# Optimization experiments

Measured on AMD Instinct MI355X. Metric: run time of the kernel, lower is better.

Reference implementation:

```python
import jax, jax.numpy as jnp
import numpy as np

N_NODES = 100000
N_EDGES = 1600000
NEG_SLOPE = 0.2
EPS = 1e-6


def setup_inputs() -> dict:
    key = jax.random.key(0)
    ks = jax.random.split(key, 14)
    s = 0.1  # weight init scale
    return {
        "x": jax.random.normal(ks[0], (N_NODES, 64), jnp.float32),
        "src": jax.random.randint(ks[1], (N_EDGES,), 0, N_NODES, jnp.int32),
        "dst": jax.random.randint(ks[2], (N_EDGES,), 0, N_NODES, jnp.int32),
        "W0": s * jax.random.normal(ks[3], (64, 128), jnp.float32),
        "al0": s * jax.random.normal(ks[4], (4, 32), jnp.float32),
        "ar0": s * jax.random.normal(ks[5], (4, 32), jnp.float32),
        "W1": s * jax.random.normal(ks[6], (128, 128), jnp.float32),
        "al1": s * jax.random.normal(ks[7], (4, 32), jnp.float32),
        "ar1": s * jax.random.normal(ks[8], (4, 32), jnp.float32),
        "resW1": s * jax.random.normal(ks[9], (128, 128), jnp.float32),
        "W2": s * jax.random.normal(ks[10], (128, 32), jnp.float32),
        "al2": s * jax.random.normal(ks[11], (1, 32), jnp.float32),
        "ar2": s * jax.random.normal(ks[12], (1, 32), jnp.float32),
        "resW2": s * jax.random.normal(ks[13], (128, 32), jnp.float32),
    }


def gat_conv(h, src, dst, W, al, ar, resW):
    """DGL-style GATConv. h: [N, Fin]; returns [N, H, D]."""
    H, D = al.shape
    feat = (h @ W).reshape(-1, H, D)                       # [N,H,D]
    el = jnp.sum(feat * al, axis=-1)                       # [N,H]
    er = jnp.sum(feat * ar, axis=-1)                       # [N,H]
    e = jax.nn.leaky_relu(el[src] + er[dst], NEG_SLOPE)    # [E,H]
    # segment softmax over destination nodes
    m = jax.ops.segment_max(e, dst, num_segments=N_NODES)  # [N,H]
    ex = jnp.exp(e - m[dst])                               # [E,H]
    denom = jax.ops.segment_sum(ex, dst, num_segments=N_NODES)
    alpha = ex / denom[dst]                                # [E,H]
    msg = alpha[:, :, None] * feat[src]                    # [E,H,D]
    rst = jax.ops.segment_sum(msg, dst, num_segments=N_NODES)  # [N,H,D]
    if resW is not None:
        rst = rst + (h @ resW).reshape(-1, H, D)
    return rst


def pairnorm_scs(x, scale=1.0):
    # 'PN-SCS' mode: scale-individually then center by original column mean
    col_mean = jnp.mean(x, axis=0)
    rownorm = jnp.sqrt(EPS + jnp.sum(x * x, axis=1, keepdims=True))
    return scale * x / rownorm - col_mean


def reference(x, src, dst, W0, al0, ar0, W1, al1, ar1, resW1, W2, al2, ar2, resW2):
    # layer 0: no residual, activation applied outside
    h = gat_conv(x, src, dst, W0, al0, ar0, None)          # [N,4,32]
    h = jax.nn.elu(h.reshape(h.shape[0], -1))              # [N,128]
    h = pairnorm_scs(h)
    # middle layer: residual + internal ELU (DGL applies activation inside),
    # then the outer loop flattens and applies ELU again
    h = jax.nn.elu(gat_conv(h, src, dst, W1, al1, ar1, resW1))  # [N,4,32]
    h = jax.nn.elu(h.reshape(h.shape[0], -1))              # [N,128]
    h = pairnorm_scs(h)
    # final layer: residual, mean over heads
    h = gat_conv(h, src, dst, W2, al2, ar2, resW2)         # [N,1,32]
    h = jnp.mean(h, axis=1)                                # [N,32]
    # dgl.mean_nodes readout on a single graph -> mean over nodes
    return jnp.mean(h, axis=0)                             # [32]
```

## Files before the change

kernel.cpp:

```cpp
#include <hip/hip_runtime.h>


typedef __attribute__((ext_vector_type(8))) short s8v;
typedef __attribute__((ext_vector_type(4))) float f4v;
typedef __attribute__((ext_vector_type(2))) float f2v;
typedef __attribute__((ext_vector_type(2))) _Float16 h2;
typedef __attribute__((ext_vector_type(4))) _Float16 h4;

__device__ __forceinline__ unsigned short f2bf(float f) {
  unsigned int x = __float_as_uint(f);
  x += 0x7fffu + ((x >> 16) & 1u);
  return (unsigned short)(x >> 16);
}
__device__ __forceinline__ float bf2f(unsigned short u) {
  return __uint_as_float(((unsigned int)u) << 16);
}
__device__ __forceinline__ unsigned short f2h(float f) {
  _Float16 h = (_Float16)f;
  return __builtin_bit_cast(unsigned short, h);
}
__device__ __forceinline__ unsigned char f2fp8(float v) {
  return (unsigned char)(__builtin_amdgcn_cvt_pk_fp8_f32(v, v, 0, false) & 0xff);
}
__device__ __forceinline__ float lrelu(float x) { return fmaxf(x, 0.2f * x); }
__device__ __forceinline__ float elu1(float x) { return x > 0.f ? x : __expf(x) - 1.f; }

__device__ __forceinline__ void pack_one(const float* W, const float* al, const float* ar,
                                         const float* resW, unsigned short* out,
                                         int K, int M, int BF, int H, int RES0, int t) {
  int c = t / K, k = t - c * K;
  float v = 0.f;
  if (c < BF) {
    v = W[k * BF + c];
  } else if (c < BF + H) {
    int h = c - BF;
    float s = 0.f;
    for (int d = 0; d < 32; d++) s += W[k * BF + h * 32 + d] * al[h * 32 + d];
    v = s;
  } else if (c < BF + 2 * H) {
    int h = c - BF - H;
    float s = 0.f;
    for (int d = 0; d < 32; d++) s += W[k * BF + h * 32 + d] * ar[h * 32 + d];
    v = s;
  } else if (c >= RES0) {
    v = resW[k * (M - RES0) + (c - RES0)];
  }
  unsigned short hi = f2bf(v);
  out[c * K + k] = hi;
  out[M * K + c * K + k] = f2bf(v - bf2f(hi));
}

__global__ __launch_bounds__(256) void hist_pack_k(const int* __restrict__ dst, int* __restrict__ counts,
                                                   int* __restrict__ bhist, int E, int NB, int chunk, int P2B,
                                                   const float* __restrict__ W0, const float* __restrict__ al0,
                                                   const float* __restrict__ ar0,
                                                   const float* __restrict__ W1, const float* __restrict__ al1,
                                                   const float* __restrict__ ar1, const float* __restrict__ resW1,
                                                   const float* __restrict__ W2, const float* __restrict__ al2,
                                                   const float* __restrict__ ar2, const float* __restrict__ resW2,
                                                   unsigned short* __restrict__ w0t, unsigned short* __restrict__ w1t,
                                                   unsigned short* __restrict__ w2t) {
  if ((int)blockIdx.x < P2B) {
    __shared__ int h[512];
    for (int b = threadIdx.x; b < NB; b += 256) h[b] = 0;
    __syncthreads();
    int e0 = blockIdx.x * chunk;
    int e1 = min(E, e0 + chunk);
    for (int e = e0 + threadIdx.x; e < e1; e += 256) {
      int d = dst[e];
      atomicAdd(&counts[d], 1);
      atomicAdd(&h[d >> 8], 1);
    }
    __syncthreads();
    for (int b = threadIdx.x; b < NB; b += 256)
      bhist[(size_t)b * P2B + blockIdx.x] = h[b];
  } else {
    const int n0 = 144 * 64, n1 = 272 * 128, n2 = 80 * 128;
    int t = ((int)blockIdx.x - P2B) * 256 + threadIdx.x;
    if (t < n0) {
      pack_one(W0, al0, ar0, nullptr, w0t, 64, 144, 128, 4, 144, t);
    } else if (t < n0 + n1) {
      pack_one(W1, al1, ar1, resW1, w1t, 128, 272, 128, 4, 144, t - n0);
    } else if (t < n0 + n1 + n2) {
      pack_one(W2, al2, ar2, resW2, w2t, 128, 80, 32, 1, 48, t - n0 - n1);
    }
  }
}

__global__ __launch_bounds__(256) void scanA(const int* __restrict__ counts, int* __restrict__ rsp,
                                             int* __restrict__ bsumA, int* __restrict__ bhist,
                                             int* __restrict__ bsumB, int NA, int NSEG, int nbA) {
  __shared__ int s[256];
  int t = threadIdx.x;
  bool isA = (int)blockIdx.x < nbA;
  int bb = isA ? (int)blockIdx.x : (int)blockIdx.x - nbA;
  const int* in = isA ? counts : bhist;
  int* out = isA ? rsp : bhist;
  int* bs = isA ? bsumA : bsumB;
  int Nn = isA ? NA : NSEG;
  int base = bb * 1024 + t * 4;
  int v0 = (base + 0 < Nn) ? in[base + 0] : 0;
  int v1 = (base + 1 < Nn) ? in[base + 1] : 0;
  int v2 = (base + 2 < Nn) ? in[base + 2] : 0;
  int v3 = (base + 3 < Nn) ? in[base + 3] : 0;
  if (isA) {
    v0 = (v0 + 15) & ~15;
    v1 = (v1 + 15) & ~15;
    v2 = (v2 + 15) & ~15;
    v3 = (v3 + 15) & ~15;
  }
  s[t] = v0 + v1 + v2 + v3;
  __syncthreads();
  for (int off = 1; off < 256; off <<= 1) {
    int xv = (t >= off) ? s[t - off] : 0;
    __syncthreads();
    s[t] += xv;
    __syncthreads();
  }
  int excl = t ? s[t - 1] : 0;
  if (t == 255) bs[bb] = s[255];
  if (base + 0 < Nn) { out[base + 0] = excl; excl += v0; }
  if (base + 1 < Nn) { out[base + 1] = excl; excl += v1; }
  if (base + 2 < Nn) { out[base + 2] = excl; excl += v2; }
  if (base + 3 < Nn) { out[base + 3] = excl; }
}

__global__ __launch_bounds__(256) void scanB(int* __restrict__ rsp, const int* __restrict__ bsumA,
                                             int* __restrict__ bhist, const int* __restrict__ bsumB,
                                             int NA, int NSEG, int nbA, int nbB) {
  __shared__ int s[256];
  int t = threadIdx.x;
  bool isA = (int)blockIdx.x < nbA;
  int bb = isA ? (int)blockIdx.x : (int)blockIdx.x - nbA;
  int* arr = isA ? rsp : bhist;
  const int* bs = isA ? bsumA : bsumB;
  int nb = isA ? nbA : nbB;
  int Nn = isA ? NA : NSEG;
  s[t] = (t < nb) ? bs[t] : 0;
  __syncthreads();
  for (int off = 1; off < 256; off <<= 1) {
    int xv = (t >= off) ? s[t - off] : 0;
    __syncthreads();
    s[t] += xv;
    __syncthreads();
  }
  int pref = bb ? s[bb - 1] : 0;
  if (pref != 0) {
    int base = bb * 1024 + t * 4;
    if (base + 0 < Nn) arr[base + 0] += pref;
    if (base + 1 < Nn) arr[base + 1] += pref;
    if (base + 2 < Nn) arr[base + 2] += pref;
    if (base + 3 < Nn) arr[base + 3] += pref;
  }
}

__global__ __launch_bounds__(256) void bscatter_k(const int* __restrict__ src, const int* __restrict__ dst,
                                                  const int* __restrict__ seg, unsigned int* __restrict__ ebuf,
                                                  int E, int NB, int chunk) {
  __shared__ int cur[512];
  for (int b = threadIdx.x; b < NB; b += 256)
    cur[b] = seg[(size_t)b * gridDim.x + blockIdx.x];
  __syncthreads();
  int e0 = blockIdx.x * chunk;
  int e1 = min(E, e0 + chunk);
  for (int e = e0 + threadIdx.x; e < e1; e += 256) {
    int d = dst[e];
    int pos = atomicAdd(&cur[d >> 8], 1);
    ebuf[pos] = ((unsigned int)src[e] << 8) | (unsigned int)(d & 255);
  }
}

__global__ __launch_bounds__(256) void fscatter_k(const unsigned int* __restrict__ ebuf,
                                                  const int* __restrict__ seg,
                                                  const int* __restrict__ rsp, int* __restrict__ csr_src,
                                                  int E, int NB, int P2B, int Nn) {
  __shared__ int cur[256];
  int b = blockIdx.x;
  int node0 = b << 8;
  int node = node0 + threadIdx.x;
  if (node < Nn) cur[threadIdx.x] = rsp[node];
  __syncthreads();
  int bstart = seg[(size_t)b * P2B];
  int bend = (b + 1 < NB) ? seg[(size_t)(b + 1) * P2B] : E;
  for (int e = bstart + threadIdx.x; e < bend; e += 256) {
    unsigned int sd = ebuf[e];
    int pos = atomicAdd(&cur[sd & 255u], 1);
    csr_src[pos] = (int)(sd >> 8);
  }
}

template <int K, int M, int R, int BF, int H, int RES0, bool AF32, bool CMW>
__global__ __launch_bounds__(256) void gemm_bf16(const void* __restrict__ Av,
                                                 const unsigned short* __restrict__ Bt,
                                                 const float* __restrict__ colsum, float invN,
                                                 unsigned char* __restrict__ feat8,
                                                 float* __restrict__ el, float* __restrict__ er,
                                                 unsigned short* __restrict__ resh, int nRowTiles) {
  __shared__ float cmw_s[M];
  if constexpr (CMW) {
    for (int cc = threadIdx.x; cc < M; cc += 256) {
      float s = 0.f;
      for (int k = 0; k < K; k++)
        s += colsum[k] * (bf2f(Bt[cc * K + k]) + bf2f(Bt[(size_t)M * K + cc * K + k]));
      cmw_s[cc] = s * invN;
    }
    __syncthreads();
  }
  int wv = (int)((blockIdx.x * blockDim.x + threadIdx.x) >> 6);
  int tile0 = wv * R;
  if (tile0 >= nRowTiles) return;
  int lane = threadIdx.x & 63;
  int r = lane & 15, q = lane >> 4;
  s8v afrag[R][K / 32];
#pragma unroll
  for (int rr = 0; rr < R; rr++) {
    if constexpr (AF32) {
      const float* arow = (const float*)Av + (size_t)((tile0 + rr) * 16 + r) * K + q * 8;
#pragma unroll
      for (int kk = 0; kk < K / 32; kk++) {
        s8v v;
#pragma unroll
        for (int j = 0; j < 8; j++) v[j] = (short)f2bf(arow[kk * 32 + j]);
        afrag[rr][kk] = v;
      }
    } else {
      const unsigned short* arow = (const unsigned short*)Av + (size_t)((tile0 + rr) * 16 + r) * K + q * 8;
#pragma unroll
      for (int kk = 0; kk < K / 32; kk++) afrag[rr][kk] = *(const s8v*)(arow + kk * 32);
    }
  }
#pragma unroll
  for (int ct = 0; ct < M / 16; ct++) {
    const unsigned short* brow = Bt + (size_t)(ct * 16 + r) * K + q * 8;
    s8v bhi[K / 32], blo[K / 32];
#pragma unroll
    for (int kk = 0; kk < K / 32; kk++) {
      bhi[kk] = *(const s8v*)(brow + kk * 32);
      blo[kk] = *(const s8v*)(brow + (size_t)M * K + kk * 32);
    }
    int col = ct * 16 + r;
    float cmwv = 0.f;
    if constexpr (CMW) cmwv = cmw_s[col];
#pragma unroll
    for (int rr = 0; rr < R; rr++) {
      f4v acc = {0.f, 0.f, 0.f, 0.f};
#pragma unroll
      for (int kk = 0; kk < K / 32; kk++) {
        acc = __builtin_amdgcn_mfma_f32_16x16x32_bf16(afrag[rr][kk], bhi[kk], acc, 0, 0, 0);
        acc = __builtin_amdgcn_mfma_f32_16x16x32_bf16(afrag[rr][kk], blo[kk], acc, 0, 0, 0);
      }
      int row0 = (tile0 + rr) * 16 + q * 4;
#pragma unroll
      for (int i = 0; i < 4; i++) {
        float v = acc[i] - cmwv;
        size_t row = (size_t)(row0 + i);
        if (col < BF) {
          feat8[row * BF + col] = f2fp8(v);
        } else if (col < BF + H) {
          el[row * H + (col - BF)] = v;
        } else if (col < BF + 2 * H) {
          er[row * H + (col - BF - H)] = v;
        } else if (RES0 < M && col >= RES0) {
          resh[row * (M - RES0) + (col - RES0)] = f2h(v);
        }
      }
    }
  }
}

template <int MODE>
__global__ __launch_bounds__(256) void aggregate4(const unsigned char* __restrict__ feat8,
                                                  const float* __restrict__ el4,
                                                  const float* __restrict__ er4,
                                                  const int* __restrict__ csr_src,
                                                  const int* __restrict__ rsp,
                                                  const int* __restrict__ counts,
                                                  const unsigned short* __restrict__ resh,
                                                  unsigned short* __restrict__ vbf,
                                                  float* __restrict__ rnrm, int Nn) {
  int n = (int)((blockIdx.x * blockDim.x + threadIdx.x) >> 6);
  if (n >= Nn) return;
  int lane = threadIdx.x & 63;
  int start = __builtin_amdgcn_readfirstlane(rsp[n]);
  int deg = __builtin_amdgcn_readfirstlane(counts[n]);
  int chunks = (deg + 15) >> 4;
  int slot = lane >> 2, h = lane & 3;
  float ern = er4[(size_t)n * 4 + h];
  int hl = lane >> 4;
  unsigned dby = (unsigned)lane << 1;
  f2v a01 = {0.f, 0.f};
  float dsum = 0.f;
  float elv = el4[(size_t)csr_src[start + slot] * 4 + h];
  for (int c = 0; c < chunks; c++) {
    const int* csp = csr_src + start + (c << 4);
    int sj[16];
#pragma unroll
    for (int j = 0; j < 16; j++) sj[j] = csp[j];
    float e = elv + ern;
    float exv = (((c << 4) + slot) < deg) ? __expf(fmaxf(e, 0.2f * e)) : 0.f;
    dsum += exv;
    if (c + 1 < chunks) elv = el4[(size_t)csp[16 + slot] * 4 + h];
#pragma unroll
    for (int j = 0; j < 16; j++) {
      float aw = __shfl(exv, (j << 2) | hl);
      unsigned short u = *(const unsigned short*)(feat8 + (((unsigned)sj[j] << 7) + dby));
      f2v fv = __builtin_amdgcn_cvt_pk_f32_fp8((int)u, false);
      f2v aw2 = {aw, aw};
      a01 = __builtin_elementwise_fma(fv, aw2, a01);
    }
  }
#pragma unroll
  for (int off = 4; off < 64; off <<= 1) dsum += __shfl_xor(dsum, off);
  float inv = dsum > 0.f ? 1.f / dsum : 0.f;
  float invh = __shfl(inv, hl);
  float v0, v1;
  if (MODE == 1) {
    h2 rr = *(const h2*)(resh + (size_t)n * 128 + lane * 2);
    v0 = elu1(elu1(a01[0] * invh + (float)rr[0]));
    v1 = elu1(elu1(a01[1] * invh + (float)rr[1]));
  } else {
    v0 = elu1(a01[0] * invh);
    v1 = elu1(a01[1] * invh);
  }
  float ss = v0 * v0 + v1 * v1;
#pragma unroll
  for (int off = 1; off < 64; off <<= 1) ss += __shfl_xor(ss, off);
  float rn = sqrtf(1e-6f + ss);
  float ri = 1.f / rn;
  unsigned int pk = (unsigned int)f2bf(v0 * ri) | ((unsigned int)f2bf(v1 * ri) << 16);
  *(unsigned int*)((char*)vbf + ((size_t)n << 8) + (lane << 2)) = pk;
  if (lane == 0) rnrm[n] = rn;
}

__global__ __launch_bounds__(256) void aggregate1(const unsigned char* __restrict__ feat8,
                                                  const float* __restrict__ el1,
                                                  const float* __restrict__ er1,
                                                  const int* __restrict__ csr_src,
                                                  const int* __restrict__ rsp,
                                                  const int* __restrict__ counts,
                                                  const unsigned short* __restrict__ res2h,
                                                  float* __restrict__ out2, int Nn) {
  int n = (int)((blockIdx.x * blockDim.x + threadIdx.x) >> 6);
  if (n >= Nn) return;
  int lane = threadIdx.x & 63;
  int start = __builtin_amdgcn_readfirstlane(rsp[n]);
  int deg = __builtin_amdgcn_readfirstlane(counts[n]);
  int chunks = (deg + 15) >> 4;
  int l16 = lane & 15;
  float ern = er1[n];
  int g = lane >> 3;
  unsigned dofs4 = (unsigned)(lane & 7) << 2;
  f2v acc01 = {0.f, 0.f}, acc23 = {0.f, 0.f};
  float dsum = 0.f;
  int sA = csr_src[start + l16];
  float elv = el1[sA];
  for (int c = 0; c < chunks; c++) {
    const int* csp = csr_src + start + (c << 4);
    float exv = (((c << 4) + l16) < deg) ? __expf(lrelu(elv + ern)) : 0.f;
    dsum += exv;
    int sAc = sA;
    if (c + 1 < chunks) {
      sA = csp[16 + l16];
      elv = el1[sA];
    }
#pragma unroll
    for (int t = 0; t < 2; t++) {
      int j = (t << 3) + g;
      int sj = __shfl(sAc, j);
      float aw = __shfl(exv, j);
      f2v aw2 = {aw, aw};
      unsigned int u = *(const unsigned int*)(feat8 + (((unsigned)sj << 5) + dofs4));
      f2v fa = __builtin_amdgcn_cvt_pk_f32_fp8((int)u, false);
      f2v fb = __builtin_amdgcn_cvt_pk_f32_fp8((int)u, true);
      acc01 = __builtin_elementwise_fma(fa, aw2, acc01);
      acc23 = __builtin_elementwise_fma(fb, aw2, acc23);
    }
  }
#pragma unroll
  for (int off = 1; off < 16; off <<= 1) dsum += __shfl_xor(dsum, off);
  float inv = dsum > 0.f ? 1.f / dsum : 0.f;
#pragma unroll
  for (int off = 8; off < 64; off <<= 1) {
    acc01[0] += __shfl_xor(acc01[0], off);
    acc01[1] += __shfl_xor(acc01[1], off);
    acc23[0] += __shfl_xor(acc23[0], off);
    acc23[1] += __shfl_xor(acc23[1], off);
  }
  if (lane < 8) {
    h4 rr = *(const h4*)(res2h + (size_t)n * 32 + (lane << 2));
    float4 o;
    o.x = acc01[0] * inv + (float)rr[0];
    o.y = acc01[1] * inv + (float)rr[1];
    o.z = acc23[0] * inv + (float)rr[2];
    o.w = acc23[1] * inv + (float)rr[3];
    *(float4*)(out2 + (size_t)n * 32 + (lane << 2)) = o;
  }
}

__global__ __launch_bounds__(256) void colsum_k(const unsigned short* __restrict__ vbf,
                                                const float* __restrict__ rnrm,
                                                float* __restrict__ colsum, int Nn) {
  __shared__ float ls[256];
  int tid = threadIdx.x;
  int c = tid & 127, rsub = tid >> 7;
  float cs = 0.f;
  for (int r = blockIdx.x * 2 + rsub; r < Nn; r += gridDim.x * 2)
    cs += bf2f(vbf[(size_t)r * 128 + c]) * rnrm[r];
  ls[tid] = cs;
  __syncthreads();
  if (tid < 128) atomicAdd(&colsum[tid], ls[tid] + ls[tid + 128]);
}

__global__ __launch_bounds__(256) void final_reduce(const float* __restrict__ out2,
                                                    float* __restrict__ outsum, int Nn) {
  __shared__ float ls[32];
  if (threadIdx.x < 32) ls[threadIdx.x] = 0.f;
  __syncthreads();
  int d = threadIdx.x & 31, rl = threadIdx.x >> 5;
  float acc = 0.f;
  for (int n = blockIdx.x * 8 + rl; n < Nn; n += gridDim.x * 8)
    acc += out2[(size_t)n * 32 + d];
  atomicAdd(&ls[d], acc);
  __syncthreads();
  if (threadIdx.x < 32) atomicAdd(&outsum[threadIdx.x], ls[threadIdx.x]);
}

__global__ void finalize_k(const float* __restrict__ outsum, float* __restrict__ out, float invN) {
  int t = threadIdx.x;
  if (t < 32) out[t] = outsum[t] * invN;
}

extern "C" void kernel_launch(void* const* d_in, const int* in_sizes, int n_in,
                              void* d_out, int out_size, void* d_ws, size_t ws_size,
                              hipStream_t stream) {
  const float* x     = (const float*)d_in[0];
  const int*   src   = (const int*)d_in[1];
  const int*   dst   = (const int*)d_in[2];
  const float* W0    = (const float*)d_in[3];
  const float* al0   = (const float*)d_in[4];
  const float* ar0   = (const float*)d_in[5];
  const float* W1    = (const float*)d_in[6];
  const float* al1   = (const float*)d_in[7];
  const float* ar1   = (const float*)d_in[8];
  const float* resW1 = (const float*)d_in[9];
  const float* W2    = (const float*)d_in[10];
  const float* al2   = (const float*)d_in[11];
  const float* ar2   = (const float*)d_in[12];
  const float* resW2 = (const float*)d_in[13];
  const int N = in_sizes[0] / 64;
  const int E = in_sizes[1];
  const float invN = 1.f / (float)N;
  const int Emax = E + 15 * N + 1024;
  const int NB = (N + 255) >> 8;
  const int P2B = 512;
  const int chunk = (E + P2B - 1) / P2B;
  const int segN = NB * P2B;
  const int nbA = (N + 1023) / 1024;
  const int nbB = (segN + 1023) / 1024;

  char* p = (char*)d_ws;
  auto alloc = [&](size_t bytes) { char* r = p; p += (bytes + 255) & ~(size_t)255; return r; };

  char* zbase = p;
  int*   counts  = (int*)alloc((size_t)4 * N);
  float* colsumA = (float*)alloc(512);
  float* colsumB = (float*)alloc(512);
  float* outsum  = (float*)alloc(128);
  size_t zbytes = (size_t)(p - zbase);

  int* rsp   = (int*)alloc((size_t)4 * N);
  int* bsumA = (int*)alloc(1024);
  int* bhist = (int*)alloc((size_t)4 * segN);
  int* bsumB = (int*)alloc(1024);
  unsigned int* ebuf = (unsigned int*)alloc((size_t)4 * E);
  int* csr_src = (int*)alloc((size_t)4 * Emax);
  unsigned char*  feat8 = (unsigned char*)alloc((size_t)N * 128);
  unsigned short* vbf   = (unsigned short*)alloc((size_t)2 * N * 128);
  unsigned short* resh  = (unsigned short*)alloc((size_t)2 * N * 128);
  unsigned short* w0t = (unsigned short*)alloc((size_t)2 * 2 * 144 * 64);
  unsigned short* w1t = (unsigned short*)alloc((size_t)2 * 2 * 272 * 128);
  unsigned short* w2t = (unsigned short*)alloc((size_t)2 * 2 * 80 * 128);
  float* el4  = (float*)alloc((size_t)16 * N);
  float* er4  = (float*)alloc((size_t)16 * N);
  float* rnrm = (float*)alloc((size_t)4 * N);
  float* out2 = (float*)alloc((size_t)4 * N * 32);

  hipMemsetAsync(zbase, 0, zbytes, stream);
  hipMemsetAsync(csr_src, 0, (size_t)4 * Emax, stream);

  const int packTot = 144 * 64 + 272 * 128 + 80 * 128;
  const int packBlocks = (packTot + 255) / 256;
  hist_pack_k<<<P2B + packBlocks, 256, 0, stream>>>(dst, counts, bhist, E, NB, chunk, P2B,
                                                    W0, al0, ar0, W1, al1, ar1, resW1,
                                                    W2, al2, ar2, resW2, w0t, w1t, w2t);
  scanA<<<nbA + nbB, 256, 0, stream>>>(counts, rsp, bsumA, bhist, bsumB, N, segN, nbA);
  scanB<<<nbA + nbB, 256, 0, stream>>>(rsp, bsumA, bhist, bsumB, N, segN, nbA, nbB);
  bscatter_k<<<P2B, 256, 0, stream>>>(src, dst, bhist, ebuf, E, NB, chunk);
  fscatter_k<<<NB, 256, 0, stream>>>(ebuf, bhist, rsp, csr_src, E, NB, P2B, N);

  const int rowTiles = N / 16;
  const int gblocks = (rowTiles / 5 + 3) / 4;
  const int aggblocks = (N + 3) / 4;

  gemm_bf16<64, 144, 5, 128, 4, 144, true, false><<<gblocks, 256, 0, stream>>>(
      x, w0t, nullptr, invN, feat8, el4, er4, nullptr, rowTiles);
  aggregate4<0><<<aggblocks, 256, 0, stream>>>(feat8, el4, er4, csr_src, rsp, counts, nullptr, vbf, rnrm, N);
  colsum_k<<<512, 256, 0, stream>>>(vbf, rnrm, colsumA, N);

  gemm_bf16<128, 272, 5, 128, 4, 144, false, true><<<gblocks, 256, 0, stream>>>(
      vbf, w1t, colsumA, invN, feat8, el4, er4, resh, rowTiles);
  aggregate4<1><<<aggblocks, 256, 0, stream>>>(feat8, el4, er4, csr_src, rsp, counts, resh, vbf, rnrm, N);
  colsum_k<<<512, 256, 0, stream>>>(vbf, rnrm, colsumB, N);

  gemm_bf16<128, 80, 5, 32, 1, 48, false, true><<<gblocks, 256, 0, stream>>>(
      vbf, w2t, colsumB, invN, feat8, el4, er4, resh, rowTiles);
  aggregate1<<<aggblocks, 256, 0, stream>>>(feat8, el4, er4, csr_src, rsp, counts, resh, out2, N);
  final_reduce<<<512, 256, 0, stream>>>(out2, outsum, N);
  finalize_k<<<1, 64, 0, stream>>>(outsum, (float*)d_out, invN);
}
```

Baseline: 546.1 us.

## Derive per-node counts and offsets in fine scatter, drop global atomics and padding

Removes the per-edge global atomic on per-node counts from the histogram kernel. Each fine-scatter block now builds its own local node histogram and scan, then writes counts and row starts itself. The per-node 16-padding of CSR rows and the node-level scan are gone, so the CSR buffer shrinks and the full memset becomes a small tail memset. Separately, the GEMM row-tiles-per-block template parameter drops from 5 to 1, which launches more blocks. The risk is that the aggregation kernels may have relied on 16-aligned row starts or padded zero entries.

```diff
diff --git a/kernel.cpp b/kernel.cpp
--- a/kernel.cpp
+++ b/kernel.cpp
@@ -50,7 +50,7 @@
   out[M * K + c * K + k] = f2bf(v - bf2f(hi));
 }
 
-__global__ __launch_bounds__(256) void hist_pack_k(const int* __restrict__ dst, int* __restrict__ counts,
+__global__ __launch_bounds__(256) void hist_pack_k(const int* __restrict__ dst,
                                                    int* __restrict__ bhist, int E, int NB, int chunk, int P2B,
                                                    const float* __restrict__ W0, const float* __restrict__ al0,
                                                    const float* __restrict__ ar0,
@@ -66,11 +66,7 @@
     __syncthreads();
     int e0 = blockIdx.x * chunk;
     int e1 = min(E, e0 + chunk);
-    for (int e = e0 + threadIdx.x; e < e1; e += 256) {
-      int d = dst[e];
-      atomicAdd(&counts[d], 1);
-      atomicAdd(&h[d >> 8], 1);
-    }
+    for (int e = e0 + threadIdx.x; e < e1; e += 256) atomicAdd(&h[dst[e] >> 8], 1);
     __syncthreads();
     for (int b = threadIdx.x; b < NB; b += 256)
       bhist[(size_t)b * P2B + blockIdx.x] = h[b];
@@ -87,28 +83,14 @@
   }
 }
 
-__global__ __launch_bounds__(256) void scanA(const int* __restrict__ counts, int* __restrict__ rsp,
-                                             int* __restrict__ bsumA, int* __restrict__ bhist,
-                                             int* __restrict__ bsumB, int NA, int NSEG, int nbA) {
+__global__ __launch_bounds__(256) void pscan1(int* __restrict__ arr, int* __restrict__ bsum, int Nn) {
   __shared__ int s[256];
   int t = threadIdx.x;
-  bool isA = (int)blockIdx.x < nbA;
-  int bb = isA ? (int)blockIdx.x : (int)blockIdx.x - nbA;
-  const int* in = isA ? counts : bhist;
-  int* out = isA ? rsp : bhist;
-  int* bs = isA ? bsumA : bsumB;
-  int Nn = isA ? NA : NSEG;
-  int base = bb * 1024 + t * 4;
-  int v0 = (base + 0 < Nn) ? in[base + 0] : 0;
-  int v1 = (base + 1 < Nn) ? in[base + 1] : 0;
-  int v2 = (base + 2 < Nn) ? in[base + 2] : 0;
-  int v3 = (base + 3 < Nn) ? in[base + 3] : 0;
-  if (isA) {
-    v0 = (v0 + 15) & ~15;
-    v1 = (v1 + 15) & ~15;
-    v2 = (v2 + 15) & ~15;
-    v3 = (v3 + 15) & ~15;
-  }
+  int base = blockIdx.x * 1024 + t * 4;
+  int v0 = (base + 0 < Nn) ? arr[base + 0] : 0;
+  int v1 = (base + 1 < Nn) ? arr[base + 1] : 0;
+  int v2 = (base + 2 < Nn) ? arr[base + 2] : 0;
+  int v3 = (base + 3 < Nn) ? arr[base + 3] : 0;
   s[t] = v0 + v1 + v2 + v3;
   __syncthreads();
   for (int off = 1; off < 256; off <<= 1) {
@@ -118,25 +100,18 @@
     __syncthreads();
   }
   int excl = t ? s[t - 1] : 0;
-  if (t == 255) bs[bb] = s[255];
-  if (base + 0 < Nn) { out[base + 0] = excl; excl += v0; }
-  if (base + 1 < Nn) { out[base + 1] = excl; excl += v1; }
-  if (base + 2 < Nn) { out[base + 2] = excl; excl += v2; }
-  if (base + 3 < Nn) { out[base + 3] = excl; }
-}
-
-__global__ __launch_bounds__(256) void scanB(int* __restrict__ rsp, const int* __restrict__ bsumA,
-                                             int* __restrict__ bhist, const int* __restrict__ bsumB,
-                                             int NA, int NSEG, int nbA, int nbB) {
+  if (t == 255) bsum[blockIdx.x] = s[255];
+  if (base + 0 < Nn) { arr[base + 0] = excl; excl += v0; }
+  if (base + 1 < Nn) { arr[base + 1] = excl; excl += v1; }
+  if (base + 2 < Nn) { arr[base + 2] = excl; excl += v2; }
+  if (base + 3 < Nn) { arr[base + 3] = excl; }
+}
+
+__global__ __launch_bounds__(256) void pscan2(int* __restrict__ arr, const int* __restrict__ bsum,
+                                              int Nn, int nb) {
   __shared__ int s[256];
   int t = threadIdx.x;
-  bool isA = (int)blockIdx.x < nbA;
-  int bb = isA ? (int)blockIdx.x : (int)blockIdx.x - nbA;
-  int* arr = isA ? rsp : bhist;
-  const int* bs = isA ? bsumA : bsumB;
-  int nb = isA ? nbA : nbB;
-  int Nn = isA ? NA : NSEG;
-  s[t] = (t < nb) ? bs[t] : 0;
+  s[t] = (t < nb) ? bsum[t] : 0;
   __syncthreads();
   for (int off = 1; off < 256; off <<= 1) {
     int xv = (t >= off) ? s[t - off] : 0;
@@ -144,6 +119,7 @@
     s[t] += xv;
     __syncthreads();
   }
+  int bb = blockIdx.x;
   int pref = bb ? s[bb - 1] : 0;
   if (pref != 0) {
     int base = bb * 1024 + t * 4;
@@ -172,17 +148,36 @@
 
 __global__ __launch_bounds__(256) void fscatter_k(const unsigned int* __restrict__ ebuf,
                                                   const int* __restrict__ seg,
-                                                  const int* __restrict__ rsp, int* __restrict__ csr_src,
+                                                  int* __restrict__ csr_src,
+                                                  int* __restrict__ counts, int* __restrict__ rsp,
                                                   int E, int NB, int P2B, int Nn) {
+  __shared__ int cnt[256];
+  __shared__ int sc[256];
   __shared__ int cur[256];
   int b = blockIdx.x;
-  int node0 = b << 8;
-  int node = node0 + threadIdx.x;
-  if (node < Nn) cur[threadIdx.x] = rsp[node];
+  int t = threadIdx.x;
+  cnt[t] = 0;
   __syncthreads();
   int bstart = seg[(size_t)b * P2B];
   int bend = (b + 1 < NB) ? seg[(size_t)(b + 1) * P2B] : E;
-  for (int e = bstart + threadIdx.x; e < bend; e += 256) {
+  for (int e = bstart + t; e < bend; e += 256)
+    atomicAdd(&cnt[ebuf[e] & 255u], 1);
+  __syncthreads();
+  int v = cnt[t];
+  sc[t] = v;
+  __syncthreads();
+  for (int off = 1; off < 256; off <<= 1) {
+    int xv = (t >= off) ? sc[t - off] : 0;
+    __syncthreads();
+    sc[t] += xv;
+    __syncthreads();
+  }
+  int base = bstart + (t ? sc[t - 1] : 0);
+  int node = (b << 8) + t;
+  if (node < Nn) { counts[node] = v; rsp[node] = base; }
+  cur[t] = base;
+  __syncthreads();
+  for (int e = bstart + t; e < bend; e += 256) {
     unsigned int sd = ebuf[e];
     int pos = atomicAdd(&cur[sd & 255u], 1);
     csr_src[pos] = (int)(sd >> 8);
@@ -450,28 +445,26 @@
   const int N = in_sizes[0] / 64;
   const int E = in_sizes[1];
   const float invN = 1.f / (float)N;
-  const int Emax = E + 15 * N + 1024;
+  const int Emax = E + 64;
   const int NB = (N + 255) >> 8;
   const int P2B = 512;
   const int chunk = (E + P2B - 1) / P2B;
   const int segN = NB * P2B;
-  const int nbA = (N + 1023) / 1024;
   const int nbB = (segN + 1023) / 1024;
 
   char* p = (char*)d_ws;
   auto alloc = [&](size_t bytes) { char* r = p; p += (bytes + 255) & ~(size_t)255; return r; };
 
   char* zbase = p;
-  int*   counts  = (int*)alloc((size_t)4 * N);
   float* colsumA = (float*)alloc(512);
   float* colsumB = (float*)alloc(512);
   float* outsum  = (float*)alloc(128);
   size_t zbytes = (size_t)(p - zbase);
 
-  int* rsp   = (int*)alloc((size_t)4 * N);
-  int* bsumA = (int*)alloc(1024);
-  int* bhist = (int*)alloc((size_t)4 * segN);
-  int* bsumB = (int*)alloc(1024);
+  int* counts = (int*)alloc((size_t)4 * N);
+  int* rsp    = (int*)alloc((size_t)4 * N);
+  int* bsumB  = (int*)alloc(1024);
+  int* bhist  = (int*)alloc((size_t)4 * segN);
   unsigned int* ebuf = (unsigned int*)alloc((size_t)4 * E);
   int* csr_src = (int*)alloc((size_t)4 * Emax);
   unsigned char*  feat8 = (unsigned char*)alloc((size_t)N * 128);
@@ -486,33 +479,33 @@
   float* out2 = (float*)alloc((size_t)4 * N * 32);
 
   hipMemsetAsync(zbase, 0, zbytes, stream);
-  hipMemsetAsync(csr_src, 0, (size_t)4 * Emax, stream);
+  hipMemsetAsync(csr_src + E, 0, (size_t)4 * (Emax - E), stream);
 
   const int packTot = 144 * 64 + 272 * 128 + 80 * 128;
   const int packBlocks = (packTot + 255) / 256;
-  hist_pack_k<<<P2B + packBlocks, 256, 0, stream>>>(dst, counts, bhist, E, NB, chunk, P2B,
+  hist_pack_k<<<P2B + packBlocks, 256, 0, stream>>>(dst, bhist, E, NB, chunk, P2B,
                                                     W0, al0, ar0, W1, al1, ar1, resW1,
                                                     W2, al2, ar2, resW2, w0t, w1t, w2t);
-  scanA<<<nbA + nbB, 256, 0, stream>>>(counts, rsp, bsumA, bhist, bsumB, N, segN, nbA);
-  scanB<<<nbA + nbB, 256, 0, stream>>>(rsp, bsumA, bhist, bsumB, N, segN, nbA, nbB);
+  pscan1<<<nbB, 256, 0, stream>>>(bhist, bsumB, segN);
+  pscan2<<<nbB, 256, 0, stream>>>(bhist, bsumB, segN, nbB);
   bscatter_k<<<P2B, 256, 0, stream>>>(src, dst, bhist, ebuf, E, NB, chunk);
-  fscatter_k<<<NB, 256, 0, stream>>>(ebuf, bhist, rsp, csr_src, E, NB, P2B, N);
+  fscatter_k<<<NB, 256, 0, stream>>>(ebuf, bhist, csr_src, counts, rsp, E, NB, P2B, N);
 
   const int rowTiles = N / 16;
-  const int gblocks = (rowTiles / 5 + 3) / 4;
+  const int gblocks = (rowTiles + 3) / 4;
   const int aggblocks = (N + 3) / 4;
 
-  gemm_bf16<64, 144, 5, 128, 4, 144, true, false><<<gblocks, 256, 0, stream>>>(
+  gemm_bf16<64, 144, 1, 128, 4, 144, true, false><<<gblocks, 256, 0, stream>>>(
       x, w0t, nullptr, invN, feat8, el4, er4, nullptr, rowTiles);
   aggregate4<0><<<aggblocks, 256, 0, stream>>>(feat8, el4, er4, csr_src, rsp, counts, nullptr, vbf, rnrm, N);
   colsum_k<<<512, 256, 0, stream>>>(vbf, rnrm, colsumA, N);
 
-  gemm_bf16<128, 272, 5, 128, 4, 144, false, true><<<gblocks, 256, 0, stream>>>(
+  gemm_bf16<128, 272, 1, 128, 4, 144, false, true><<<gblocks, 256, 0, stream>>>(
       vbf, w1t, colsumA, invN, feat8, el4, er4, resh, rowTiles);
   aggregate4<1><<<aggblocks, 256, 0, stream>>>(feat8, el4, er4, csr_src, rsp, counts, resh, vbf, rnrm, N);
   colsum_k<<<512, 256, 0, stream>>>(vbf, rnrm, colsumB, N);
 
-  gemm_bf16<128, 80, 5, 32, 1, 48, false, true><<<gblocks, 256, 0, stream>>>(
+  gemm_bf16<128, 80, 1, 32, 1, 48, false, true><<<gblocks, 256, 0, stream>>>(
       vbf, w2t, colsumB, invN, feat8, el4, er4, resh, rowTiles);
   aggregate1<<<aggblocks, 256, 0, stream>>>(feat8, el4, er4, csr_src, rsp, counts, resh, out2, N);
   final_reduce<<<512, 256, 0, stream>>>(out2, outsum, N);
```

Result: slower. 613.6 us (+12.4%).
